# Kernel tuning notes

Measured on AMD Instinct MI355X. Metric: run time of the kernel, lower is better.

Reference implementation:

```python
import jax, jax.numpy as jnp
import numpy as np

B, S, DIM = 2, 1024, 1024
E, K, INTER = 16, 2, 512
SHARED_INTER = 2 * INTER  # n_shared_experts * moe_inter_dim
ROUTE_SCALE = 1.0


def setup_inputs() -> dict:
    key = jax.random.key(0)
    ks = jax.random.split(key, 8)
    init = lambda k, shape: jax.random.normal(k, shape, dtype=jnp.float32) * 0.02
    return {
        "x": jax.random.normal(ks[0], (B, S, DIM), dtype=jnp.float32),
        "gate_w": init(ks[1], (E, DIM)),
        "w1": init(ks[2], (E, INTER, DIM)),
        "w2": init(ks[3], (E, DIM, INTER)),
        "w3": init(ks[4], (E, INTER, DIM)),
        "sw1": init(ks[5], (SHARED_INTER, DIM)),
        "sw2": init(ks[6], (DIM, SHARED_INTER)),
        "sw3": init(ks[7], (SHARED_INTER, DIM)),
    }


def reference(x, gate_w, w1, w2, w3, sw1, sw2, sw3):
    b, s, d = x.shape
    xt = x.reshape(-1, d)            # [T, D] flattened tokens
    T = xt.shape[0]

    # Gate: sigmoid scores, top-k experts, normalize selected weights
    scores = jax.nn.sigmoid(xt @ gate_w.T)           # [T, E]
    topv, topi = jax.lax.top_k(scores, K)            # [T, K]
    weights = topv / jnp.sum(topv, axis=-1, keepdims=True) * ROUTE_SCALE

    # Per-token dense combine weights over experts: gate[t, e]
    gate = jnp.zeros((T, E), xt.dtype).at[jnp.arange(T)[:, None], topi].add(weights)

    # Routed experts (SwiGLU), computed densely and combined with gate weights
    h = jax.nn.silu(jnp.einsum('td,eid->tei', xt, w1)) * jnp.einsum('td,eid->tei', xt, w3)
    expert_out = jnp.einsum('tei,edi->ted', h, w2)   # [T, E, D]
    y = jnp.einsum('ted,te->td', expert_out, gate)   # [T, D]

    # Shared expert (SwiGLU MLP over all tokens)
    z = (jax.nn.silu(xt @ sw1.T) * (xt @ sw3.T)) @ sw2.T

    return (y + z).reshape(b, s, d)
```

## Files before the change

kernel.cpp:

```cpp
#include <hip/hip_runtime.h>
#include <stdint.h>

typedef unsigned short u16;
typedef __bf16 bf16x8 __attribute__((ext_vector_type(8)));
typedef float f32x4 __attribute__((ext_vector_type(4)));
typedef unsigned short u16x8 __attribute__((ext_vector_type(8)));

#define TTOK 2048
#define DIMSZ 1024
#define NROUT 16
#define INTERSZ 512

__device__ __forceinline__ u16 f2bf(float f) {
    unsigned int u = __builtin_bit_cast(unsigned int, f);
    unsigned int r = u + 0x7FFFu + ((u >> 16) & 1u);
    return (u16)(r >> 16);
}

__device__ __forceinline__ void gl2lds16(const void* g, void* l) {
    __builtin_amdgcn_global_load_lds(
        (const __attribute__((address_space(1))) void*)(uintptr_t)g,
        (__attribute__((address_space(3))) void*)(uintptr_t)l,
        16, 0, 0);
}

#define NA4 (NROUT * INTERSZ * DIMSZ / 4)
#define NB4 (DIMSZ * DIMSZ / 4)
#define NA8 (NA4 / 2)
#define NR8 ((NA4 + NB4) / 2)
__global__ __launch_bounds__(256) void prep(
    const float* __restrict__ w1, const float* __restrict__ sw1,
    const float* __restrict__ w3, const float* __restrict__ sw3,
    const float* __restrict__ w2, const float* __restrict__ sw2,
    u16* __restrict__ W1b, u16* __restrict__ W3b, u16* __restrict__ W2b,
    const float* __restrict__ x, const float* __restrict__ gw,
    int* __restrict__ topi, float2* __restrict__ topw,
    u16* __restrict__ Xbf, float* __restrict__ out) {
    const int r = blockIdx.y;
    const int tid = threadIdx.x;
    if (r < 3) {
        const float* a; const float* b; u16* d;
        if (r == 0)      { a = w1; b = sw1; d = W1b; }
        else if (r == 1) { a = w3; b = sw3; d = W3b; }
        else             { a = w2; b = sw2; d = W2b; }
        const int stride = gridDim.x * blockDim.x;
        for (int j = blockIdx.x * blockDim.x + tid; j < NR8; j += stride) {
            const float4* src = (j < NA8) ? (const float4*)a + 2 * (size_t)j
                                          : (const float4*)b + 2 * (size_t)(j - NA8);
            float4 v0 = src[0], v1 = src[1];
            u16x8 o;
            o[0] = f2bf(v0.x); o[1] = f2bf(v0.y); o[2] = f2bf(v0.z); o[3] = f2bf(v0.w);
            o[4] = f2bf(v1.x); o[5] = f2bf(v1.y); o[6] = f2bf(v1.z); o[7] = f2bf(v1.w);
            *(u16x8*)&d[(size_t)j * 8] = o;
        }
        return;
    }
    const int t = blockIdx.x;
    const int wave = tid >> 6, lane = tid & 63;
    const int d0 = tid * 4;
    *(float4*)(out + (size_t)t * DIMSZ + d0) = make_float4(0.f, 0.f, 0.f, 0.f);
    float4 xv = *(const float4*)(x + (size_t)t * DIMSZ + d0);
    ushort4 o;
    o.x = f2bf(xv.x); o.y = f2bf(xv.y); o.z = f2bf(xv.z); o.w = f2bf(xv.w);
    *(ushort4*)&Xbf[(size_t)t * DIMSZ + d0] = o;

    float acc[16];
    #pragma unroll
    for (int e = 0; e < 16; ++e) {
        float4 g = *(const float4*)(gw + e * DIMSZ + d0);
        acc[e] = xv.x * g.x + xv.y * g.y + xv.z * g.z + xv.w * g.w;
    }
    #pragma unroll
    for (int off = 32; off > 0; off >>= 1) {
        #pragma unroll
        for (int e = 0; e < 16; ++e) acc[e] += __shfl_xor(acc[e], off);
    }
    __shared__ float part[4][16];
    __shared__ float sfin[16];
    if (lane < 16) part[wave][lane] = acc[lane];
    __syncthreads();
    if (wave == 0 && lane < 16) {
        float s = part[0][lane] + part[1][lane] + part[2][lane] + part[3][lane];
        sfin[lane] = 1.f / (1.f + expf(-s));
    }
    __syncthreads();
    if (tid == 0) {
        int i0 = 0; float v0 = sfin[0];
        #pragma unroll
        for (int e = 1; e < 16; ++e) { float v = sfin[e]; if (v > v0) { v0 = v; i0 = e; } }
        int i1 = -1; float v1 = -1e30f;
        #pragma unroll
        for (int e = 0; e < 16; ++e) { float v = sfin[e]; if (e != i0 && v > v1) { v1 = v; i1 = e; } }
        float inv = 1.f / (v0 + v1);
        topi[t] = i0 | (i1 << 8);
        topw[t] = make_float2(v0 * inv, v1 * inv);
    }
}

__global__ __launch_bounds__(256) void route_kernel(
    const int* __restrict__ topi, const float2* __restrict__ topw,
    int* __restrict__ counts, int* __restrict__ tokidx, float* __restrict__ tokw) {
    const int e = blockIdx.x;
    const int tid = threadIdx.x;
    int p[8]; int m[8]; int cnt = 0;
    #pragma unroll
    for (int j = 0; j < 8; ++j) {
        int t = tid * 8 + j;
        p[j] = topi[t];
        m[j] = ((p[j] & 255) == e) || ((p[j] >> 8) == e) ? 1 : 0;
        cnt += m[j];
    }
    const int lane = tid & 63, wave = tid >> 6;
    int v = cnt;
    #pragma unroll
    for (int off = 1; off < 64; off <<= 1) {
        int u = __shfl_up(v, off);
        if (lane >= off) v += u;
    }
    __shared__ int wsum[4];
    if (lane == 63) wsum[wave] = v;
    __syncthreads();
    int wbase = 0;
    #pragma unroll
    for (int w = 0; w < 4; ++w) wbase += (w < wave) ? wsum[w] : 0;
    int base = wbase + v - cnt;
    #pragma unroll
    for (int j = 0; j < 8; ++j) {
        if (m[j]) {
            int t = tid * 8 + j;
            float2 w2 = topw[t];
            tokidx[e * TTOK + base] = t;
            tokw[e * TTOK + base] = ((p[j] & 255) == e) ? w2.x : w2.y;
            ++base;
        }
    }
    if (tid == 0) counts[e] = wsum[0] + wsum[1] + wsum[2] + wsum[3];
}

__global__ __launch_bounds__(256) void gemm1s(
    const u16* __restrict__ Xbf, const u16* __restrict__ W1b,
    const u16* __restrict__ W3b, const int* __restrict__ counts,
    const int* __restrict__ tokidx, const float* __restrict__ tokw,
    u16* __restrict__ Hc, u16* __restrict__ Hs) {
    const int e = blockIdx.z;
    const int cnt = (e < NROUT) ? counts[e] : TTOK;
    const int m0 = blockIdx.y * 64;
    if (m0 >= cnt) return;
    const int n0 = blockIdx.x * 128;
    __shared__ u16 As[64 * 64], B1s[128 * 64], B3s[128 * 64];
    const size_t eoff = (size_t)e * INTERSZ * DIMSZ;
    const u16* B1 = W1b + eoff + (size_t)n0 * DIMSZ;
    const u16* B3 = W3b + eoff + (size_t)n0 * DIMSZ;
    const int tid = threadIdx.x;

    int rowa[2], cgsa[2]; size_t arow[2];
    #pragma unroll
    for (int i = 0; i < 2; ++i) {
        int c = tid + i * 256;
        rowa[i] = c >> 3;
        cgsa[i] = ((c & 7) ^ (rowa[i] & 7)) * 8;
        int slot = m0 + rowa[i];
        int g;
        if (e < NROUT) g = (slot < cnt) ? tokidx[e * TTOK + slot] : 0;
        else           g = slot;
        arow[i] = (size_t)g * DIMSZ;
    }
    int rowb[4], cgsb[4];
    #pragma unroll
    for (int i = 0; i < 4; ++i) {
        int c = tid + i * 256;
        rowb[i] = c >> 3;
        cgsb[i] = ((c & 7) ^ (rowb[i] & 7)) * 8;
    }
    f32x4 acc1[2][4] = {}; f32x4 acc3[2][4] = {};
    const int wave = tid >> 6, lane = tid & 63;
    const int wm = (wave >> 1) * 32, wn = (wave & 1) * 64;
    const int lr = lane & 15, lq = lane >> 4;

    for (int kt = 0; kt < DIMSZ / 64; ++kt) {
        const int k0 = kt * 64;
        #pragma unroll
        for (int i = 0; i < 2; ++i) {
            int c = tid + i * 256;
            gl2lds16(Xbf + arow[i] + k0 + cgsa[i], &As[c * 8]);
        }
        #pragma unroll
        for (int i = 0; i < 4; ++i) {
            int c = tid + i * 256;
            int boff = rowb[i] * DIMSZ + k0 + cgsb[i];
            gl2lds16(B1 + boff, &B1s[c * 8]);
            gl2lds16(B3 + boff, &B3s[c * 8]);
        }
        __syncthreads();
        #pragma unroll
        for (int ks = 0; ks < 2; ++ks) {
            bf16x8 af[2], b1f[4], b3f[4];
            const int g = lq + ks * 4;
            #pragma unroll
            for (int mt = 0; mt < 2; ++mt) {
                int m = wm + mt * 16 + lr;
                af[mt] = *(const bf16x8*)&As[(m * 8 + (g ^ (m & 7))) * 8];
            }
            #pragma unroll
            for (int nt = 0; nt < 4; ++nt) {
                int n = wn + nt * 16 + lr;
                int ch = (n * 8 + (g ^ (n & 7))) * 8;
                b1f[nt] = *(const bf16x8*)&B1s[ch];
                b3f[nt] = *(const bf16x8*)&B3s[ch];
            }
            #pragma unroll
            for (int mt = 0; mt < 2; ++mt) {
                #pragma unroll
                for (int nt = 0; nt < 4; ++nt) {
                    acc1[mt][nt] = __builtin_amdgcn_mfma_f32_16x16x32_bf16(af[mt], b1f[nt], acc1[mt][nt], 0, 0, 0);
                    acc3[mt][nt] = __builtin_amdgcn_mfma_f32_16x16x32_bf16(af[mt], b3f[nt], acc3[mt][nt], 0, 0, 0);
                }
            }
        }
        __syncthreads();
    }
    #pragma unroll
    for (int mt = 0; mt < 2; ++mt) {
        #pragma unroll
        for (int nt = 0; nt < 4; ++nt) {
            #pragma unroll
            for (int r = 0; r < 4; ++r) {
                int m = wm + mt * 16 + lq * 4 + r;
                int n = wn + nt * 16 + lr;
                int slot = m0 + m;
                bool valid = slot < cnt;
                float h1 = acc1[mt][nt][r], h3 = acc3[mt][nt][r];
                float hv = 0.f;
                if (valid) {
                    float tw = (e < NROUT) ? tokw[e * TTOK + slot] : 1.0f;
                    hv = h1 / (1.f + __expf(-h1)) * h3 * tw;
                }
                if (e < NROUT)
                    Hc[((size_t)e * TTOK + slot) * INTERSZ + n0 + n] = f2bf(hv);
                else
                    Hs[(size_t)slot * DIMSZ + (e - NROUT) * INTERSZ + n0 + n] = f2bf(hv);
            }
        }
    }
}

__global__ __launch_bounds__(256) void gemm2u(
    const u16* __restrict__ Hc, const u16* __restrict__ Hs,
    const u16* __restrict__ W2b, const u16* __restrict__ W2sb,
    const int* __restrict__ counts, const int* __restrict__ tokidx,
    float* __restrict__ out) {
    const int e = blockIdx.z;
    const bool routed = (e < NROUT);
    const int cnt = routed ? counts[e] : TTOK;
    const int m0 = blockIdx.y * 64;
    if (m0 >= cnt) return;
    const int n0 = blockIdx.x * 128;
    const int klen = routed ? INTERSZ : DIMSZ;
    __shared__ u16 As[64 * 64], Bs[128 * 64];
    const u16* A0 = routed ? Hc + ((size_t)e * TTOK + m0) * INTERSZ
                           : Hs + (size_t)m0 * DIMSZ;
    const u16* B0 = routed ? W2b + ((size_t)e * DIMSZ + n0) * INTERSZ
                           : W2sb + (size_t)n0 * DIMSZ;
    const int tid = threadIdx.x;
    const int wave = tid >> 6, lane = tid & 63;
    const int wm = (wave >> 1) * 32, wn = (wave & 1) * 64;
    const int lr = lane & 15, lq = lane >> 4;

    int rowa[2], cgsa[2];
    #pragma unroll
    for (int i = 0; i < 2; ++i) {
        int c = tid + i * 256;
        rowa[i] = c >> 3;
        cgsa[i] = ((c & 7) ^ (rowa[i] & 7)) * 8;
    }
    int rowb[4], cgsb[4];
    #pragma unroll
    for (int i = 0; i < 4; ++i) {
        int c = tid + i * 256;
        rowb[i] = c >> 3;
        cgsb[i] = ((c & 7) ^ (rowb[i] & 7)) * 8;
    }

    f32x4 acc[2][4] = {};
    for (int kt = 0; kt < klen / 64; ++kt) {
        const int k0 = kt * 64;
        #pragma unroll
        for (int i = 0; i < 2; ++i) {
            int c = tid + i * 256;
            gl2lds16(A0 + (size_t)rowa[i] * klen + k0 + cgsa[i], &As[c * 8]);
        }
        #pragma unroll
        for (int i = 0; i < 4; ++i) {
            int c = tid + i * 256;
            gl2lds16(B0 + (size_t)rowb[i] * klen + k0 + cgsb[i], &Bs[c * 8]);
        }
        __syncthreads();
        #pragma unroll
        for (int ks = 0; ks < 2; ++ks) {
            bf16x8 af[2], bfr[4];
            const int g = lq + ks * 4;
            #pragma unroll
            for (int mt = 0; mt < 2; ++mt) {
                int m = wm + mt * 16 + lr;
                af[mt] = *(const bf16x8*)&As[(m * 8 + (g ^ (m & 7))) * 8];
            }
            #pragma unroll
            for (int nt = 0; nt < 4; ++nt) {
                int n = wn + nt * 16 + lr;
                bfr[nt] = *(const bf16x8*)&Bs[(n * 8 + (g ^ (n & 7))) * 8];
            }
            #pragma unroll
            for (int mt = 0; mt < 2; ++mt) {
                #pragma unroll
                for (int nt = 0; nt < 4; ++nt) {
                    acc[mt][nt] = __builtin_amdgcn_mfma_f32_16x16x32_bf16(af[mt], bfr[nt], acc[mt][nt], 0, 0, 0);
                }
            }
        }
        __syncthreads();
    }
    #pragma unroll
    for (int mt = 0; mt < 2; ++mt) {
        #pragma unroll
        for (int r = 0; r < 4; ++r) {
            int m = wm + mt * 16 + lq * 4 + r;
            int slot = m0 + m;
            if (slot < cnt) {
                int t = routed ? tokidx[e * TTOK + slot] : slot;
                #pragma unroll
                for (int nt = 0; nt < 4; ++nt) {
                    int n = wn + nt * 16 + lr;
                    unsafeAtomicAdd(&out[(size_t)t * DIMSZ + n0 + n], acc[mt][nt][r]);
                }
            }
        }
    }
}

extern "C" void kernel_launch(void* const* d_in, const int* in_sizes, int n_in,
                              void* d_out, int out_size, void* d_ws, size_t ws_size,
                              hipStream_t stream) {
    const float* x      = (const float*)d_in[0];
    const float* gate_w = (const float*)d_in[1];
    const float* w1     = (const float*)d_in[2];
    const float* w2     = (const float*)d_in[3];
    const float* w3     = (const float*)d_in[4];
    const float* sw1    = (const float*)d_in[5];
    const float* sw2    = (const float*)d_in[6];
    const float* sw3    = (const float*)d_in[7];
    float* out = (float*)d_out;

    char* ws = (char*)d_ws;
    const size_t SZ_W   = (size_t)(NROUT + 2) * INTERSZ * DIMSZ * 2;
    const size_t SZ_XBF = (size_t)TTOK * DIMSZ * 2;
    u16*   W1b    = (u16*)(ws);
    u16*   W3b    = (u16*)(ws + SZ_W);
    u16*   W2all  = (u16*)(ws + 2 * SZ_W);
    u16*   Xbf    = (u16*)(ws + 3 * SZ_W);
    char*  route  = ws + 3 * SZ_W + SZ_XBF;
    int*   counts = (int*)route;
    int*   topi   = (int*)(route + 256);
    float2* topw  = (float2*)(route + 256 + TTOK * 4);
    int*   tokidx = (int*)(route + 256 + TTOK * 12);
    float* tokw   = (float*)(route + 256 + TTOK * 12 + 16 * TTOK * 4);
    char*  hbuf   = route + 256 + TTOK * 12 + 2 * (size_t)16 * TTOK * 4;
    u16*   Hc     = (u16*)hbuf;
    u16*   Hs     = (u16*)(hbuf + (size_t)NROUT * TTOK * INTERSZ * 2);
    u16*   W2sb   = W2all + (size_t)NROUT * DIMSZ * INTERSZ;

    prep<<<dim3(2048, 4), 256, 0, stream>>>(
        w1, sw1, w3, sw3, w2, sw2, W1b, W3b, W2all,
        x, gate_w, topi, topw, Xbf, out);
    route_kernel<<<NROUT, 256, 0, stream>>>(topi, topw, counts, tokidx, tokw);
    gemm1s<<<dim3(INTERSZ / 128, TTOK / 64, NROUT + 2), 256, 0, stream>>>(
        Xbf, W1b, W3b, counts, tokidx, tokw, Hc, Hs);
    gemm2u<<<dim3(DIMSZ / 128, TTOK / 64, NROUT + 1), 256, 0, stream>>>(
        Hc, Hs, W2all, W2sb, counts, tokidx, out);
}
```

Baseline: 231.2 us.

## Move w2 bf16 cast into gemm1 launch and batch cast loads per thread

The fp32-to-bf16 conversion of w2/sw2 moves out of the prep kernel into an extra z-slice of the gemm1 grid, so it can overlap with the first-stage expert GEMMs instead of running before routing. The remaining w1/w3 cast in prep now uses a fixed block count, and each thread issues several independent loads before converting, raising memory-level parallelism. The cost is extra cast blocks competing with GEMM blocks for CUs and bandwidth, and index math that hardcodes the grid shape.

```diff
diff --git a/kernel.cpp b/kernel.cpp
--- a/kernel.cpp
+++ b/kernel.cpp
@@ -28,30 +28,41 @@
 #define NB4 (DIMSZ * DIMSZ / 4)
 #define NA8 (NA4 / 2)
 #define NR8 ((NA4 + NB4) / 2)
+#define CAST_BLKS 1152
+
 __global__ __launch_bounds__(256) void prep(
     const float* __restrict__ w1, const float* __restrict__ sw1,
     const float* __restrict__ w3, const float* __restrict__ sw3,
-    const float* __restrict__ w2, const float* __restrict__ sw2,
-    u16* __restrict__ W1b, u16* __restrict__ W3b, u16* __restrict__ W2b,
+    u16* __restrict__ W1b, u16* __restrict__ W3b,
     const float* __restrict__ x, const float* __restrict__ gw,
     int* __restrict__ topi, float2* __restrict__ topw,
     u16* __restrict__ Xbf, float* __restrict__ out) {
     const int r = blockIdx.y;
     const int tid = threadIdx.x;
-    if (r < 3) {
-        const float* a; const float* b; u16* d;
-        if (r == 0)      { a = w1; b = sw1; d = W1b; }
-        else if (r == 1) { a = w3; b = sw3; d = W3b; }
-        else             { a = w2; b = sw2; d = W2b; }
-        const int stride = gridDim.x * blockDim.x;
-        for (int j = blockIdx.x * blockDim.x + tid; j < NR8; j += stride) {
-            const float4* src = (j < NA8) ? (const float4*)a + 2 * (size_t)j
-                                          : (const float4*)b + 2 * (size_t)(j - NA8);
-            float4 v0 = src[0], v1 = src[1];
+    if (r < 2) {
+        if (blockIdx.x >= CAST_BLKS) return;
+        const float* a = r ? w3 : w1;
+        const float* b = r ? sw3 : sw1;
+        u16* d = r ? W3b : W1b;
+        float4 v[8];
+        size_t js[4];
+        #pragma unroll
+        for (int k = 0; k < 4; ++k) {
+            size_t j = (size_t)blockIdx.x * 1024 + k * 256 + tid;
+            js[k] = j;
+            const float4* src = (j < NA8) ? (const float4*)a + 2 * j
+                                          : (const float4*)b + 2 * (j - NA8);
+            v[2 * k]     = src[0];
+            v[2 * k + 1] = src[1];
+        }
+        #pragma unroll
+        for (int k = 0; k < 4; ++k) {
             u16x8 o;
-            o[0] = f2bf(v0.x); o[1] = f2bf(v0.y); o[2] = f2bf(v0.z); o[3] = f2bf(v0.w);
-            o[4] = f2bf(v1.x); o[5] = f2bf(v1.y); o[6] = f2bf(v1.z); o[7] = f2bf(v1.w);
-            *(u16x8*)&d[(size_t)j * 8] = o;
+            o[0] = f2bf(v[2 * k].x);     o[1] = f2bf(v[2 * k].y);
+            o[2] = f2bf(v[2 * k].z);     o[3] = f2bf(v[2 * k].w);
+            o[4] = f2bf(v[2 * k + 1].x); o[5] = f2bf(v[2 * k + 1].y);
+            o[6] = f2bf(v[2 * k + 1].z); o[7] = f2bf(v[2 * k + 1].w);
+            *(u16x8*)&d[js[k] * 8] = o;
         }
         return;
     }
@@ -141,8 +152,38 @@
     const u16* __restrict__ Xbf, const u16* __restrict__ W1b,
     const u16* __restrict__ W3b, const int* __restrict__ counts,
     const int* __restrict__ tokidx, const float* __restrict__ tokw,
-    u16* __restrict__ Hc, u16* __restrict__ Hs) {
+    u16* __restrict__ Hc, u16* __restrict__ Hs,
+    const float* __restrict__ w2f, const float* __restrict__ sw2f,
+    u16* __restrict__ W2c) {
     const int e = blockIdx.z;
+    const int tid = threadIdx.x;
+    if (e == NROUT + 2) {
+        const int bid = blockIdx.y * gridDim.x + blockIdx.x;
+        #pragma unroll
+        for (int it = 0; it < 9; ++it) {
+            float4 v[8];
+            size_t js[4];
+            #pragma unroll
+            for (int k = 0; k < 4; ++k) {
+                size_t j = (size_t)bid * 9216 + it * 1024 + k * 256 + tid;
+                js[k] = j;
+                const float4* src = (j < NA8) ? (const float4*)w2f + 2 * j
+                                              : (const float4*)sw2f + 2 * (j - NA8);
+                v[2 * k]     = src[0];
+                v[2 * k + 1] = src[1];
+            }
+            #pragma unroll
+            for (int k = 0; k < 4; ++k) {
+                u16x8 o;
+                o[0] = f2bf(v[2 * k].x);     o[1] = f2bf(v[2 * k].y);
+                o[2] = f2bf(v[2 * k].z);     o[3] = f2bf(v[2 * k].w);
+                o[4] = f2bf(v[2 * k + 1].x); o[5] = f2bf(v[2 * k + 1].y);
+                o[6] = f2bf(v[2 * k + 1].z); o[7] = f2bf(v[2 * k + 1].w);
+                *(u16x8*)&W2c[js[k] * 8] = o;
+            }
+        }
+        return;
+    }
     const int cnt = (e < NROUT) ? counts[e] : TTOK;
     const int m0 = blockIdx.y * 64;
     if (m0 >= cnt) return;
@@ -151,7 +192,6 @@
     const size_t eoff = (size_t)e * INTERSZ * DIMSZ;
     const u16* B1 = W1b + eoff + (size_t)n0 * DIMSZ;
     const u16* B3 = W3b + eoff + (size_t)n0 * DIMSZ;
-    const int tid = threadIdx.x;
 
     int rowa[2], cgsa[2]; size_t arow[2];
     #pragma unroll
@@ -368,12 +408,12 @@
     u16*   Hs     = (u16*)(hbuf + (size_t)NROUT * TTOK * INTERSZ * 2);
     u16*   W2sb   = W2all + (size_t)NROUT * DIMSZ * INTERSZ;
 
-    prep<<<dim3(2048, 4), 256, 0, stream>>>(
-        w1, sw1, w3, sw3, w2, sw2, W1b, W3b, W2all,
+    prep<<<dim3(2048, 3), 256, 0, stream>>>(
+        w1, sw1, w3, sw3, W1b, W3b,
         x, gate_w, topi, topw, Xbf, out);
     route_kernel<<<NROUT, 256, 0, stream>>>(topi, topw, counts, tokidx, tokw);
-    gemm1s<<<dim3(INTERSZ / 128, TTOK / 64, NROUT + 2), 256, 0, stream>>>(
-        Xbf, W1b, W3b, counts, tokidx, tokw, Hc, Hs);
+    gemm1s<<<dim3(INTERSZ / 128, TTOK / 64, NROUT + 3), 256, 0, stream>>>(
+        Xbf, W1b, W3b, counts, tokidx, tokw, Hc, Hs, w2, sw2, W2all);
     gemm2u<<<dim3(DIMSZ / 128, TTOK / 64, NROUT + 1), 256, 0, stream>>>(
         Hc, Hs, W2all, W2sb, counts, tokidx, out);
 }
```

Result: slower. 243.5 us (+5.4%).

## Convert fp32 weights to bf16 inside GEMM tiles instead of a prep pass

Applied to the files above, without the earlier changes.

Removes the separate weight-conversion pass that wrote bf16 copies of all expert and shared weights. The GEMM kernels now load fp32 weight tiles into registers, prefetching one k-step ahead, and convert them to bf16 when storing to LDS. This avoids a full read and write of the weights, but each tile re-reads fp32 weights (twice the bytes) per m-block, and the async global-to-LDS loads for B are replaced by register staging.

```diff
diff --git a/kernel.cpp b/kernel.cpp
--- a/kernel.cpp
+++ b/kernel.cpp
@@ -15,6 +15,13 @@
     unsigned int u = __builtin_bit_cast(unsigned int, f);
     unsigned int r = u + 0x7FFFu + ((u >> 16) & 1u);
     return (u16)(r >> 16);
+}
+
+__device__ __forceinline__ u16x8 cvt8(float4 a, float4 b) {
+    u16x8 o;
+    o[0] = f2bf(a.x); o[1] = f2bf(a.y); o[2] = f2bf(a.z); o[3] = f2bf(a.w);
+    o[4] = f2bf(b.x); o[5] = f2bf(b.y); o[6] = f2bf(b.z); o[7] = f2bf(b.w);
+    return o;
 }
 
 __device__ __forceinline__ void gl2lds16(const void* g, void* l) {
@@ -24,37 +31,11 @@
         16, 0, 0);
 }
 
-#define NA4 (NROUT * INTERSZ * DIMSZ / 4)
-#define NB4 (DIMSZ * DIMSZ / 4)
-#define NA8 (NA4 / 2)
-#define NR8 ((NA4 + NB4) / 2)
 __global__ __launch_bounds__(256) void prep(
-    const float* __restrict__ w1, const float* __restrict__ sw1,
-    const float* __restrict__ w3, const float* __restrict__ sw3,
-    const float* __restrict__ w2, const float* __restrict__ sw2,
-    u16* __restrict__ W1b, u16* __restrict__ W3b, u16* __restrict__ W2b,
     const float* __restrict__ x, const float* __restrict__ gw,
     int* __restrict__ topi, float2* __restrict__ topw,
     u16* __restrict__ Xbf, float* __restrict__ out) {
-    const int r = blockIdx.y;
     const int tid = threadIdx.x;
-    if (r < 3) {
-        const float* a; const float* b; u16* d;
-        if (r == 0)      { a = w1; b = sw1; d = W1b; }
-        else if (r == 1) { a = w3; b = sw3; d = W3b; }
-        else             { a = w2; b = sw2; d = W2b; }
-        const int stride = gridDim.x * blockDim.x;
-        for (int j = blockIdx.x * blockDim.x + tid; j < NR8; j += stride) {
-            const float4* src = (j < NA8) ? (const float4*)a + 2 * (size_t)j
-                                          : (const float4*)b + 2 * (size_t)(j - NA8);
-            float4 v0 = src[0], v1 = src[1];
-            u16x8 o;
-            o[0] = f2bf(v0.x); o[1] = f2bf(v0.y); o[2] = f2bf(v0.z); o[3] = f2bf(v0.w);
-            o[4] = f2bf(v1.x); o[5] = f2bf(v1.y); o[6] = f2bf(v1.z); o[7] = f2bf(v1.w);
-            *(u16x8*)&d[(size_t)j * 8] = o;
-        }
-        return;
-    }
     const int t = blockIdx.x;
     const int wave = tid >> 6, lane = tid & 63;
     const int d0 = tid * 4;
@@ -138,20 +119,25 @@
 }
 
 __global__ __launch_bounds__(256) void gemm1s(
-    const u16* __restrict__ Xbf, const u16* __restrict__ W1b,
-    const u16* __restrict__ W3b, const int* __restrict__ counts,
+    const u16* __restrict__ Xbf,
+    const float* __restrict__ w1f, const float* __restrict__ w3f,
+    const float* __restrict__ sw1f, const float* __restrict__ sw3f,
+    const int* __restrict__ counts,
     const int* __restrict__ tokidx, const float* __restrict__ tokw,
     u16* __restrict__ Hc, u16* __restrict__ Hs) {
     const int e = blockIdx.z;
+    const int tid = threadIdx.x;
     const int cnt = (e < NROUT) ? counts[e] : TTOK;
     const int m0 = blockIdx.y * 64;
     if (m0 >= cnt) return;
     const int n0 = blockIdx.x * 128;
     __shared__ u16 As[64 * 64], B1s[128 * 64], B3s[128 * 64];
-    const size_t eoff = (size_t)e * INTERSZ * DIMSZ;
-    const u16* B1 = W1b + eoff + (size_t)n0 * DIMSZ;
-    const u16* B3 = W3b + eoff + (size_t)n0 * DIMSZ;
-    const int tid = threadIdx.x;
+    const float* B1f = (e < NROUT ? w1f + (size_t)e * INTERSZ * DIMSZ
+                                  : sw1f + (size_t)(e - NROUT) * INTERSZ * DIMSZ)
+                       + (size_t)n0 * DIMSZ;
+    const float* B3f = (e < NROUT ? w3f + (size_t)e * INTERSZ * DIMSZ
+                                  : sw3f + (size_t)(e - NROUT) * INTERSZ * DIMSZ)
+                       + (size_t)n0 * DIMSZ;
 
     int rowa[2], cgsa[2]; size_t arow[2];
     #pragma unroll
@@ -176,8 +162,18 @@
     const int wave = tid >> 6, lane = tid & 63;
     const int wm = (wave >> 1) * 32, wn = (wave & 1) * 64;
     const int lr = lane & 15, lq = lane >> 4;
-
-    for (int kt = 0; kt < DIMSZ / 64; ++kt) {
+    const int NKT = DIMSZ / 64;
+
+    float4 pb1[4][2], pb3[4][2];
+    #pragma unroll
+    for (int i = 0; i < 4; ++i) {
+        const float* p1 = B1f + (size_t)rowb[i] * DIMSZ + cgsb[i];
+        const float* p3 = B3f + (size_t)rowb[i] * DIMSZ + cgsb[i];
+        pb1[i][0] = *(const float4*)p1; pb1[i][1] = *(const float4*)(p1 + 4);
+        pb3[i][0] = *(const float4*)p3; pb3[i][1] = *(const float4*)(p3 + 4);
+    }
+
+    for (int kt = 0; kt < NKT; ++kt) {
         const int k0 = kt * 64;
         #pragma unroll
         for (int i = 0; i < 2; ++i) {
@@ -187,11 +183,20 @@
         #pragma unroll
         for (int i = 0; i < 4; ++i) {
             int c = tid + i * 256;
-            int boff = rowb[i] * DIMSZ + k0 + cgsb[i];
-            gl2lds16(B1 + boff, &B1s[c * 8]);
-            gl2lds16(B3 + boff, &B3s[c * 8]);
+            *(u16x8*)&B1s[c * 8] = cvt8(pb1[i][0], pb1[i][1]);
+            *(u16x8*)&B3s[c * 8] = cvt8(pb3[i][0], pb3[i][1]);
         }
         __syncthreads();
+        if (kt + 1 < NKT) {
+            const int kn = k0 + 64;
+            #pragma unroll
+            for (int i = 0; i < 4; ++i) {
+                const float* p1 = B1f + (size_t)rowb[i] * DIMSZ + kn + cgsb[i];
+                const float* p3 = B3f + (size_t)rowb[i] * DIMSZ + kn + cgsb[i];
+                pb1[i][0] = *(const float4*)p1; pb1[i][1] = *(const float4*)(p1 + 4);
+                pb3[i][0] = *(const float4*)p3; pb3[i][1] = *(const float4*)(p3 + 4);
+            }
+        }
         #pragma unroll
         for (int ks = 0; ks < 2; ++ks) {
             bf16x8 af[2], b1f[4], b3f[4];
@@ -246,7 +251,7 @@
 
 __global__ __launch_bounds__(256) void gemm2u(
     const u16* __restrict__ Hc, const u16* __restrict__ Hs,
-    const u16* __restrict__ W2b, const u16* __restrict__ W2sb,
+    const float* __restrict__ w2f, const float* __restrict__ sw2f,
     const int* __restrict__ counts, const int* __restrict__ tokidx,
     float* __restrict__ out) {
     const int e = blockIdx.z;
@@ -259,8 +264,8 @@
     __shared__ u16 As[64 * 64], Bs[128 * 64];
     const u16* A0 = routed ? Hc + ((size_t)e * TTOK + m0) * INTERSZ
                            : Hs + (size_t)m0 * DIMSZ;
-    const u16* B0 = routed ? W2b + ((size_t)e * DIMSZ + n0) * INTERSZ
-                           : W2sb + (size_t)n0 * DIMSZ;
+    const float* B0f = routed ? w2f + (size_t)e * DIMSZ * INTERSZ + (size_t)n0 * INTERSZ
+                              : sw2f + (size_t)n0 * DIMSZ;
     const int tid = threadIdx.x;
     const int wave = tid >> 6, lane = tid & 63;
     const int wm = (wave >> 1) * 32, wn = (wave & 1) * 64;
@@ -281,8 +286,16 @@
         cgsb[i] = ((c & 7) ^ (rowb[i] & 7)) * 8;
     }
 
+    const int NKT = klen / 64;
+    float4 pb[4][2];
+    #pragma unroll
+    for (int i = 0; i < 4; ++i) {
+        const float* p = B0f + (size_t)rowb[i] * klen + cgsb[i];
+        pb[i][0] = *(const float4*)p; pb[i][1] = *(const float4*)(p + 4);
+    }
+
     f32x4 acc[2][4] = {};
-    for (int kt = 0; kt < klen / 64; ++kt) {
+    for (int kt = 0; kt < NKT; ++kt) {
         const int k0 = kt * 64;
         #pragma unroll
         for (int i = 0; i < 2; ++i) {
@@ -292,9 +305,17 @@
         #pragma unroll
         for (int i = 0; i < 4; ++i) {
             int c = tid + i * 256;
-            gl2lds16(B0 + (size_t)rowb[i] * klen + k0 + cgsb[i], &Bs[c * 8]);
+            *(u16x8*)&Bs[c * 8] = cvt8(pb[i][0], pb[i][1]);
         }
         __syncthreads();
+        if (kt + 1 < NKT) {
+            const int kn = k0 + 64;
+            #pragma unroll
+            for (int i = 0; i < 4; ++i) {
+                const float* p = B0f + (size_t)rowb[i] * klen + kn + cgsb[i];
+                pb[i][0] = *(const float4*)p; pb[i][1] = *(const float4*)(p + 4);
+            }
+        }
         #pragma unroll
         for (int ks = 0; ks < 2; ++ks) {
             bf16x8 af[2], bfr[4];
@@ -351,13 +372,9 @@
     float* out = (float*)d_out;
 
     char* ws = (char*)d_ws;
-    const size_t SZ_W   = (size_t)(NROUT + 2) * INTERSZ * DIMSZ * 2;
     const size_t SZ_XBF = (size_t)TTOK * DIMSZ * 2;
-    u16*   W1b    = (u16*)(ws);
-    u16*   W3b    = (u16*)(ws + SZ_W);
-    u16*   W2all  = (u16*)(ws + 2 * SZ_W);
-    u16*   Xbf    = (u16*)(ws + 3 * SZ_W);
-    char*  route  = ws + 3 * SZ_W + SZ_XBF;
+    u16*   Xbf    = (u16*)ws;
+    char*  route  = ws + SZ_XBF;
     int*   counts = (int*)route;
     int*   topi   = (int*)(route + 256);
     float2* topw  = (float2*)(route + 256 + TTOK * 4);
@@ -366,14 +383,11 @@
     char*  hbuf   = route + 256 + TTOK * 12 + 2 * (size_t)16 * TTOK * 4;
     u16*   Hc     = (u16*)hbuf;
     u16*   Hs     = (u16*)(hbuf + (size_t)NROUT * TTOK * INTERSZ * 2);
-    u16*   W2sb   = W2all + (size_t)NROUT * DIMSZ * INTERSZ;
-
-    prep<<<dim3(2048, 4), 256, 0, stream>>>(
-        w1, sw1, w3, sw3, w2, sw2, W1b, W3b, W2all,
-        x, gate_w, topi, topw, Xbf, out);
+
+    prep<<<dim3(2048), 256, 0, stream>>>(x, gate_w, topi, topw, Xbf, out);
     route_kernel<<<NROUT, 256, 0, stream>>>(topi, topw, counts, tokidx, tokw);
     gemm1s<<<dim3(INTERSZ / 128, TTOK / 64, NROUT + 2), 256, 0, stream>>>(
-        Xbf, W1b, W3b, counts, tokidx, tokw, Hc, Hs);
+        Xbf, w1, w3, sw1, sw3, counts, tokidx, tokw, Hc, Hs);
     gemm2u<<<dim3(DIMSZ / 128, TTOK / 64, NROUT + 1), 256, 0, stream>>>(
-        Hc, Hs, W2all, W2sb, counts, tokidx, out);
-}
+        Hc, Hs, w2, sw2, counts, tokidx, out);
+}
```

Measured after the change: 269.1 us. +16.4%, slower.
